# Optimization experiments

Measured on AMD Instinct MI355X. Metric: run time of the kernel, lower is better.

The kernel has to match this reference:

```python
import jax, jax.numpy as jnp
import numpy as np

T, D, F, FS, E = 2048, 1024, 2048, 2048, 8
TOP_K = 1


def setup_inputs() -> dict:
    key = jax.random.key(0)
    ks = jax.random.split(key, 8)
    sd = 1.0 / np.sqrt(D)
    sf = 1.0 / np.sqrt(F)
    sfs = 1.0 / np.sqrt(FS)
    return {
        "hidden_states": jax.random.normal(ks[0], (T, D), jnp.float32),
        "router_w": jax.random.normal(ks[1], (E, D), jnp.float32) * sd,     # Linear(D->E), no bias
        "w_gate": jax.random.normal(ks[2], (E, D, F), jnp.float32) * sd,    # fused gate half
        "w_up": jax.random.normal(ks[3], (E, D, F), jnp.float32) * sd,      # fused up half
        "w_down": jax.random.normal(ks[4], (E, F, D), jnp.float32) * sf,
        "ws_gate": jax.random.normal(ks[5], (D, FS), jnp.float32) * sd,
        "ws_up": jax.random.normal(ks[6], (D, FS), jnp.float32) * sd,
        "ws_down": jax.random.normal(ks[7], (FS, D), jnp.float32) * sfs,
    }


def reference(hidden_states, router_w, w_gate, w_up, w_down, ws_gate, ws_up, ws_down):
    # Router: logits -> top-k -> sigmoid of top-k values (Llama4RenormalizeMoeRoutingMethod)
    logits = hidden_states @ router_w.T                      # [T, E]
    top_vals, top_idx = jax.lax.top_k(logits, TOP_K)         # [T, K]
    scores = jax.nn.sigmoid(top_vals.astype(jnp.float32)).astype(hidden_states.dtype)
    # Combine weights [T, E]; apply_router_weight_on_input=True -> scale INPUT per routed copy
    combine = (jax.nn.one_hot(top_idx, E, dtype=hidden_states.dtype) * scores[..., None]).sum(axis=1)
    xe = combine.T[:, :, None] * hidden_states[None]          # [E, T, D] (zero for non-routed tokens)
    g = jnp.einsum('etd,edf->etf', xe, w_gate)
    u = jnp.einsum('etd,edf->etf', xe, w_up)
    routed = jnp.einsum('etf,efd->etd', jax.nn.silu(g) * u, w_down).sum(axis=0)  # [T, D]
    # Shared expert (GatedMLP, SiLU)
    shared = (jax.nn.silu(hidden_states @ ws_gate) * (hidden_states @ ws_up)) @ ws_down
    return shared + routed
```

## Files before the change

kernel.cpp:

```cpp
#include <hip/hip_runtime.h>
#include <hip/hip_bf16.h>
#include <cstdint>
#include <cstddef>

#define T_TOK 2048
#define DIM   1024
#define FDIM  2048
#define NEXP  8

#define GU_MAX 48
#define DN_MAX 64

typedef short  short8  __attribute__((ext_vector_type(8)));
typedef float  floatx4 __attribute__((ext_vector_type(4)));

__device__ inline unsigned short f2bf(float f) {
    unsigned int u = __builtin_bit_cast(unsigned int, f);
    unsigned int r = (u + 0x7FFFu + ((u >> 16) & 1u)) >> 16;
    return (unsigned short)r;
}

__device__ inline unsigned int pk2bf(float a, float b) {
    return (unsigned int)f2bf(a) | ((unsigned int)f2bf(b) << 16);
}

__device__ inline void glds16(const void* g, const unsigned short* lds_base, int elem_off) {
    int u = __builtin_amdgcn_readfirstlane(elem_off);
    __builtin_amdgcn_global_load_lds(
        (const __attribute__((address_space(1))) unsigned int*)g,
        (__attribute__((address_space(3))) unsigned int*)(lds_base + u), 16, 0, 0);
}

__global__ __launch_bounds__(256) void k_router(
    const float* __restrict__ h, const float* __restrict__ rw,
    int* __restrict__ counts, int* __restrict__ lists,
    unsigned short* __restrict__ hb, unsigned short* __restrict__ xb)
{
    int w = threadIdx.x >> 6, lane = threadIdx.x & 63;
    int t = blockIdx.x * 4 + w;
    const float* hrow = h + (size_t)t * DIM;
    float hv[16];
    #pragma unroll
    for (int i = 0; i < 16; ++i) hv[i] = hrow[lane + 64 * i];
    float acc[NEXP];
    #pragma unroll
    for (int e = 0; e < NEXP; ++e) {
        const float* r = rw + (size_t)e * DIM;
        float s = 0.f;
        #pragma unroll
        for (int i = 0; i < 16; ++i) s += hv[i] * r[lane + 64 * i];
        acc[e] = s;
    }
    #pragma unroll
    for (int e = 0; e < NEXP; ++e) {
        float s = acc[e];
        for (int off = 32; off > 0; off >>= 1) s += __shfl_down(s, off);
        acc[e] = s;
    }
    float score = 0.f;
    if (lane == 0) {
        int be = 0; float bv = acc[0];
        #pragma unroll
        for (int e = 1; e < NEXP; ++e) if (acc[e] > bv) { bv = acc[e]; be = e; }
        score = 1.f / (1.f + __expf(-bv));
        int pos = atomicAdd(&counts[be], 1);
        lists[be * T_TOK + pos] = t;
    }
    score = __shfl(score, 0);
    unsigned short* hbr = hb + (size_t)t * DIM;
    unsigned short* xbr = xb + (size_t)t * DIM;
    #pragma unroll
    for (int i = 0; i < 16; ++i) {
        hbr[lane + 64 * i] = f2bf(hv[i]);
        xbr[lane + 64 * i] = f2bf(score * hv[i]);
    }
}

__global__ void k_schedule(const int* __restrict__ counts,
                           int* __restrict__ gu, int* __restrict__ dn)
{
    if (threadIdx.x != 0 || blockIdx.x != 0) return;
    int n = 0;
    for (int e = 0; e < NEXP; ++e) {
        int c = counts[e];
        for (int r = 0; r < c; r += 128) gu[n++] = (e << 16) | r;
    }
    for (int r = 0; r < T_TOK; r += 128) gu[n++] = (NEXP << 16) | r;
    while (n < GU_MAX) gu[n++] = -1;
    n = 0;
    for (int e = 0; e < NEXP; ++e) {
        int c = counts[e];
        for (int r = 0; r < c; r += 128) {
            dn[n++] = (e << 16) | r;
            dn[n++] = (1 << 28) | (e << 16) | r;
        }
    }
    while (n < DN_MAX) dn[n++] = -1;
}

__global__ __launch_bounds__(256, 2) void k_gateup(
    const unsigned short* __restrict__ xb, const unsigned short* __restrict__ hb,
    const float* __restrict__ w_gate, const float* __restrict__ w_up,
    const float* __restrict__ ws_gate, const float* __restrict__ ws_up,
    const int* __restrict__ counts, const int* __restrict__ lists,
    const int* __restrict__ gu_tiles, unsigned short* __restrict__ Hc)
{
    int ent = gu_tiles[blockIdx.y];
    if (ent < 0) return;
    int e = ent >> 16, row0 = ent & 0xffff;
    bool sh = (e == NEXP);
    int cnt = sh ? T_TOK : counts[e];
    const unsigned short* Asrc = sh ? hb : xb;
    const float* Bg = sh ? ws_gate : w_gate + (size_t)e * DIM * FDIM;
    const float* Bu = sh ? ws_up   : w_up   + (size_t)e * DIM * FDIM;
    int outoff = sh ? FDIM : 0;
    int col0 = blockIdx.x * 128;

    __shared__ int toks[128];
    __shared__ __align__(16) unsigned short As [2][128 * 32];
    __shared__ __align__(16) unsigned short Bgs[2][128 * 32];
    __shared__ __align__(16) unsigned short Bus[2][128 * 32];

    int tid = threadIdx.x;
    if (tid < 128) {
        int r = row0 + tid;
        toks[tid] = (r < cnt) ? (sh ? r : lists[e * T_TOK + r]) : -1;
    }
    __syncthreads();

    int lane = tid & 63, w = tid >> 6;
    int wm = w >> 1, wn = w & 1;

    size_t agoff[2]; int albase[2];
    #pragma unroll
    for (int it = 0; it < 2; ++it) {
        int tt = tid + it * 256;
        int rr = tt >> 2, sq = tt & 3;
        int kg = (sq ^ ((rr >> 1) & 3)) * 8;
        int tk = toks[rr]; if (tk < 0) tk = 0;
        agoff[it] = (size_t)tk * DIM + kg;
        albase[it] = (it * 256 + w * 64) * 8;
    }

    int c = tid & 63;
    int kq = w;
    int slotB = (kq ^ (c & 3)) * 8;
    const float* bgp = Bg + (size_t)(kq * 8) * FDIM + col0 + 2 * c;
    const float* bup = Bu + (size_t)(kq * 8) * FDIM + col0 + 2 * c;

    float2 gx[8], ux[8];
    auto loadB = [&](int k0) {
        const float* pg = bgp + (size_t)k0 * FDIM;
        const float* pu = bup + (size_t)k0 * FDIM;
        #pragma unroll
        for (int j = 0; j < 8; ++j) {
            gx[j] = *(const float2*)(pg + (size_t)j * FDIM);
            ux[j] = *(const float2*)(pu + (size_t)j * FDIM);
        }
    };
    auto commitB = [&](int p) {
        unsigned int ge[4], go[4], ue[4], uo[4];
        #pragma unroll
        for (int j = 0; j < 4; ++j) {
            ge[j] = pk2bf(gx[2*j].x, gx[2*j+1].x);
            go[j] = pk2bf(gx[2*j].y, gx[2*j+1].y);
            ue[j] = pk2bf(ux[2*j].x, ux[2*j+1].x);
            uo[j] = pk2bf(ux[2*j].y, ux[2*j+1].y);
        }
        *(uint4*)&Bgs[p][(2*c)   * 32 + slotB] = make_uint4(ge[0], ge[1], ge[2], ge[3]);
        *(uint4*)&Bgs[p][(2*c+1) * 32 + slotB] = make_uint4(go[0], go[1], go[2], go[3]);
        *(uint4*)&Bus[p][(2*c)   * 32 + slotB] = make_uint4(ue[0], ue[1], ue[2], ue[3]);
        *(uint4*)&Bus[p][(2*c+1) * 32 + slotB] = make_uint4(uo[0], uo[1], uo[2], uo[3]);
    };
    auto loadA = [&](int k0, int p) {
        #pragma unroll
        for (int it = 0; it < 2; ++it)
            glds16(Asrc + agoff[it] + k0, &As[p][0], albase[it]);
    };

    floatx4 accg[4][4], accu[4][4];
    #pragma unroll
    for (int mi = 0; mi < 4; ++mi)
    #pragma unroll
    for (int ni = 0; ni < 4; ++ni) {
        floatx4 z = {0.f, 0.f, 0.f, 0.f};
        accg[mi][ni] = z; accu[mi][ni] = z;
    }

    loadA(0, 0);
    loadB(0);
    commitB(0);
    loadB(32);

    int p = 0;
    for (int k0 = 0; k0 < DIM; k0 += 32) {
        __syncthreads();
        int nk = k0 + 32;
        if (nk < DIM) {
            loadA(nk, p ^ 1);
            commitB(p ^ 1);
            if (nk + 32 < DIM) loadB(nk + 32);
        }
        int kb = (lane >> 4) * 8;
        short8 af[4], bgf[4], buf_[4];
        #pragma unroll
        for (int mi = 0; mi < 4; ++mi) {
            int r = wm * 64 + mi * 16 + (lane & 15);
            int slot = ((kb >> 3) ^ ((r >> 1) & 3)) * 8;
            af[mi] = *(const short8*)&As[p][r * 32 + slot];
        }
        #pragma unroll
        for (int ni = 0; ni < 4; ++ni) {
            int n = wn * 64 + ni * 16 + (lane & 15);
            int slot = ((kb >> 3) ^ ((n >> 1) & 3)) * 8;
            bgf[ni]  = *(const short8*)&Bgs[p][n * 32 + slot];
            buf_[ni] = *(const short8*)&Bus[p][n * 32 + slot];
        }
        #pragma unroll
        for (int mi = 0; mi < 4; ++mi)
        #pragma unroll
        for (int ni = 0; ni < 4; ++ni) {
            accg[mi][ni] = __builtin_amdgcn_mfma_f32_16x16x32_bf16(af[mi], bgf[ni],  accg[mi][ni], 0, 0, 0);
            accu[mi][ni] = __builtin_amdgcn_mfma_f32_16x16x32_bf16(af[mi], buf_[ni], accu[mi][ni], 0, 0, 0);
        }
        p ^= 1;
    }

    #pragma unroll
    for (int mi = 0; mi < 4; ++mi)
    #pragma unroll
    for (int ni = 0; ni < 4; ++ni)
    #pragma unroll
    for (int r = 0; r < 4; ++r) {
        int row = wm * 64 + mi * 16 + (lane >> 4) * 4 + r;
        int tok = toks[row];
        if (tok < 0) continue;
        int col = col0 + wn * 64 + ni * 16 + (lane & 15);
        float g = accg[mi][ni][r], u = accu[mi][ni][r];
        float hval = (g / (1.f + __expf(-g))) * u;
        Hc[(size_t)tok * (2 * FDIM) + outoff + col] = f2bf(hval);
    }
}

__global__ __launch_bounds__(256) void k_down(
    const unsigned short* __restrict__ Hc,
    const float* __restrict__ w_down, const float* __restrict__ ws_down,
    const int* __restrict__ counts, const int* __restrict__ lists,
    const int* __restrict__ dn_tiles, float* __restrict__ out)
{
    int ent = dn_tiles[blockIdx.y];
    if (ent < 0) return;
    int ks = (ent >> 28) & 1, e = (ent >> 16) & 0xff, row0 = ent & 0xffff;
    int cnt = counts[e];
    const float* B = ks ? ws_down : w_down + (size_t)e * FDIM * DIM;
    int col0 = blockIdx.x * 64;
    size_t abase = (size_t)ks * FDIM;

    __shared__ int toks[128];
    __shared__ __align__(16) unsigned short As[2][128 * 32];
    __shared__ __align__(16) unsigned short Bs[2][64 * 32];

    int tid = threadIdx.x;
    if (tid < 128) {
        int r = row0 + tid;
        toks[tid] = (r < cnt) ? lists[e * T_TOK + r] : -1;
    }
    __syncthreads();

    int lane = tid & 63, w = tid >> 6;
    int wm = w >> 1, wn = w & 1;

    size_t agoff[2]; int albase[2];
    #pragma unroll
    for (int it = 0; it < 2; ++it) {
        int tt = tid + it * 256;
        int rr = tt >> 2, sq = tt & 3;
        int kg = (sq ^ ((rr >> 1) & 3)) * 8;
        int tk = toks[rr]; if (tk < 0) tk = 0;
        agoff[it] = (size_t)tk * (2 * FDIM) + abase + kg;
        albase[it] = (it * 256 + w * 64) * 8;
    }

    int c = tid & 63;
    int kq = w;
    int slotB = (kq ^ ((c >> 1) & 3)) * 8;
    const float* bp = B + (size_t)(kq * 8) * DIM + col0 + c;

    float bx[8];
    auto loadB = [&](int k0) {
        const float* pb = bp + (size_t)k0 * DIM;
        #pragma unroll
        for (int j = 0; j < 8; ++j) bx[j] = pb[(size_t)j * DIM];
    };
    auto commitB = [&](int p) {
        unsigned int bw[4];
        #pragma unroll
        for (int j = 0; j < 4; ++j) bw[j] = pk2bf(bx[2*j], bx[2*j+1]);
        *(uint4*)&Bs[p][c * 32 + slotB] = make_uint4(bw[0], bw[1], bw[2], bw[3]);
    };
    auto loadA = [&](int k0, int p) {
        #pragma unroll
        for (int it = 0; it < 2; ++it)
            glds16(Hc + agoff[it] + k0, &As[p][0], albase[it]);
    };

    floatx4 acc[4][2];
    #pragma unroll
    for (int mi = 0; mi < 4; ++mi)
    #pragma unroll
    for (int ni = 0; ni < 2; ++ni) {
        floatx4 z = {0.f, 0.f, 0.f, 0.f};
        acc[mi][ni] = z;
    }

    loadA(0, 0);
    loadB(0);
    commitB(0);
    loadB(32);

    int p = 0;
    for (int k0 = 0; k0 < FDIM; k0 += 32) {
        __syncthreads();
        int nk = k0 + 32;
        if (nk < FDIM) {
            loadA(nk, p ^ 1);
            commitB(p ^ 1);
            if (nk + 32 < FDIM) loadB(nk + 32);
        }
        int kb = (lane >> 4) * 8;
        short8 af[4], bf[2];
        #pragma unroll
        for (int mi = 0; mi < 4; ++mi) {
            int r = wm * 64 + mi * 16 + (lane & 15);
            int slot = ((kb >> 3) ^ ((r >> 1) & 3)) * 8;
            af[mi] = *(const short8*)&As[p][r * 32 + slot];
        }
        #pragma unroll
        for (int ni = 0; ni < 2; ++ni) {
            int n = wn * 32 + ni * 16 + (lane & 15);
            int slot = ((kb >> 3) ^ ((n >> 1) & 3)) * 8;
            bf[ni] = *(const short8*)&Bs[p][n * 32 + slot];
        }
        #pragma unroll
        for (int mi = 0; mi < 4; ++mi)
        #pragma unroll
        for (int ni = 0; ni < 2; ++ni)
            acc[mi][ni] = __builtin_amdgcn_mfma_f32_16x16x32_bf16(af[mi], bf[ni], acc[mi][ni], 0, 0, 0);
        p ^= 1;
    }

    #pragma unroll
    for (int mi = 0; mi < 4; ++mi)
    #pragma unroll
    for (int ni = 0; ni < 2; ++ni)
    #pragma unroll
    for (int r = 0; r < 4; ++r) {
        int row = wm * 64 + mi * 16 + (lane >> 4) * 4 + r;
        int tok = toks[row];
        if (tok < 0) continue;
        int col = col0 + wn * 32 + ni * 16 + (lane & 15);
        atomicAdd(&out[(size_t)tok * DIM + col], acc[mi][ni][r]);
    }
}

extern "C" void kernel_launch(void* const* d_in, const int* in_sizes, int n_in,
                              void* d_out, int out_size, void* d_ws, size_t ws_size,
                              hipStream_t stream)
{
    const float* h   = (const float*)d_in[0];
    const float* rw  = (const float*)d_in[1];
    const float* wg  = (const float*)d_in[2];
    const float* wu  = (const float*)d_in[3];
    const float* wd  = (const float*)d_in[4];
    const float* wsg = (const float*)d_in[5];
    const float* wsu = (const float*)d_in[6];
    const float* wsd = (const float*)d_in[7];
    float* out = (float*)d_out;

    char* ws = (char*)d_ws;
    int* counts   = (int*)ws;
    int* gu_tiles = (int*)(ws + 256);
    int* dn_tiles = (int*)(ws + 1024);
    int* lists    = (int*)(ws + 2048);
    unsigned short* hb = (unsigned short*)(ws + 131072);
    unsigned short* xb = hb + (size_t)T_TOK * DIM;
    unsigned short* Hc = xb + (size_t)T_TOK * DIM;

    (void)hipMemsetAsync(counts, 0, 64, stream);
    (void)hipMemsetAsync(out, 0, (size_t)T_TOK * DIM * sizeof(float), stream);
    k_router<<<dim3(T_TOK / 4), 256, 0, stream>>>(h, rw, counts, lists, hb, xb);
    k_schedule<<<dim3(1), 64, 0, stream>>>(counts, gu_tiles, dn_tiles);
    k_gateup<<<dim3(FDIM / 128, GU_MAX), 256, 0, stream>>>(
        xb, hb, wg, wu, wsg, wsu, counts, lists, gu_tiles, Hc);
    k_down<<<dim3(DIM / 64, DN_MAX), 256, 0, stream>>>(
        Hc, wd, wsd, counts, lists, dn_tiles, out);
}
```

Measured before the change: 417.6 us.

## Restructure GEMM pipelines with hardware bf16 convert, padded LDS, wider down tiles

Replaces the software bf16 rounding with the v_cvt_pk_bf16_f32 instruction. The B tiles in LDS get a padded stride of 40 with a new XOR swizzle to cut bank conflicts. Both GEMM main loops are reordered: an explicit waitcnt plus barrier, the A prefetch issued first, the B commit and next load placed after the fragment reads, and s_setprio raised around the MFMA block. The down kernel's N tile grows from 64 to 128 columns with float2 B loads and launch bounds of (256,2). This raises register and LDS pressure, and the hand-tuned vmcnt values must match the exact number of outstanding loads.

Result: faster. 394.8 us (-5.5%).

```diff
diff --git a/kernel.cpp b/kernel.cpp
--- a/kernel.cpp
+++ b/kernel.cpp
@@ -20,8 +20,10 @@
     return (unsigned short)r;
 }
 
-__device__ inline unsigned int pk2bf(float a, float b) {
-    return (unsigned int)f2bf(a) | ((unsigned int)f2bf(b) << 16);
+__device__ inline unsigned int cvtpk(float a, float b) {
+    unsigned int r;
+    asm("v_cvt_pk_bf16_f32 %0, %1, %2" : "=v"(r) : "v"(a), "v"(b));
+    return r;
 }
 
 __device__ inline void glds16(const void* g, const unsigned short* lds_base, int elem_off) {
@@ -118,8 +120,8 @@
 
     __shared__ int toks[128];
     __shared__ __align__(16) unsigned short As [2][128 * 32];
-    __shared__ __align__(16) unsigned short Bgs[2][128 * 32];
-    __shared__ __align__(16) unsigned short Bus[2][128 * 32];
+    __shared__ __align__(16) unsigned short Bgs[2][128 * 40];
+    __shared__ __align__(16) unsigned short Bus[2][128 * 40];
 
     int tid = threadIdx.x;
     if (tid < 128) {
@@ -143,10 +145,9 @@
     }
 
     int c = tid & 63;
-    int kq = w;
-    int slotB = (kq ^ (c & 3)) * 8;
-    const float* bgp = Bg + (size_t)(kq * 8) * FDIM + col0 + 2 * c;
-    const float* bup = Bu + (size_t)(kq * 8) * FDIM + col0 + 2 * c;
+    int slotW = (w ^ ((c >> 2) & 1)) * 8;
+    const float* bgp = Bg + (size_t)(w * 8) * FDIM + col0 + 2 * c;
+    const float* bup = Bu + (size_t)(w * 8) * FDIM + col0 + 2 * c;
 
     float2 gx[8], ux[8];
     auto loadB = [&](int k0) {
@@ -158,24 +159,24 @@
             ux[j] = *(const float2*)(pu + (size_t)j * FDIM);
         }
     };
-    auto commitB = [&](int p) {
+    auto commitB = [&](int p_) {
         unsigned int ge[4], go[4], ue[4], uo[4];
         #pragma unroll
         for (int j = 0; j < 4; ++j) {
-            ge[j] = pk2bf(gx[2*j].x, gx[2*j+1].x);
-            go[j] = pk2bf(gx[2*j].y, gx[2*j+1].y);
-            ue[j] = pk2bf(ux[2*j].x, ux[2*j+1].x);
-            uo[j] = pk2bf(ux[2*j].y, ux[2*j+1].y);
-        }
-        *(uint4*)&Bgs[p][(2*c)   * 32 + slotB] = make_uint4(ge[0], ge[1], ge[2], ge[3]);
-        *(uint4*)&Bgs[p][(2*c+1) * 32 + slotB] = make_uint4(go[0], go[1], go[2], go[3]);
-        *(uint4*)&Bus[p][(2*c)   * 32 + slotB] = make_uint4(ue[0], ue[1], ue[2], ue[3]);
-        *(uint4*)&Bus[p][(2*c+1) * 32 + slotB] = make_uint4(uo[0], uo[1], uo[2], uo[3]);
-    };
-    auto loadA = [&](int k0, int p) {
+            ge[j] = cvtpk(gx[2*j].x, gx[2*j+1].x);
+            go[j] = cvtpk(gx[2*j].y, gx[2*j+1].y);
+            ue[j] = cvtpk(ux[2*j].x, ux[2*j+1].x);
+            uo[j] = cvtpk(ux[2*j].y, ux[2*j+1].y);
+        }
+        *(uint4*)&Bgs[p_][(2*c)   * 40 + slotW] = make_uint4(ge[0], ge[1], ge[2], ge[3]);
+        *(uint4*)&Bgs[p_][(2*c+1) * 40 + slotW] = make_uint4(go[0], go[1], go[2], go[3]);
+        *(uint4*)&Bus[p_][(2*c)   * 40 + slotW] = make_uint4(ue[0], ue[1], ue[2], ue[3]);
+        *(uint4*)&Bus[p_][(2*c+1) * 40 + slotW] = make_uint4(uo[0], uo[1], uo[2], uo[3]);
+    };
+    auto loadA = [&](int k0, int p_) {
         #pragma unroll
         for (int it = 0; it < 2; ++it)
-            glds16(Asrc + agoff[it] + k0, &As[p][0], albase[it]);
+            glds16(Asrc + agoff[it] + k0, &As[p_][0], albase[it]);
     };
 
     floatx4 accg[4][4], accu[4][4];
@@ -194,28 +195,31 @@
 
     int p = 0;
     for (int k0 = 0; k0 < DIM; k0 += 32) {
-        __syncthreads();
-        int nk = k0 + 32;
-        if (nk < DIM) {
-            loadA(nk, p ^ 1);
-            commitB(p ^ 1);
-            if (nk + 32 < DIM) loadB(nk + 32);
-        }
-        int kb = (lane >> 4) * 8;
+        asm volatile("s_waitcnt vmcnt(16) lgkmcnt(0)\n\ts_barrier" ::: "memory");
+        bool more = (k0 + 32 < DIM);
+        if (more) loadA(k0 + 32, p ^ 1);
+        __builtin_amdgcn_sched_barrier(0);
+        int g = lane >> 4;
         short8 af[4], bgf[4], buf_[4];
         #pragma unroll
         for (int mi = 0; mi < 4; ++mi) {
             int r = wm * 64 + mi * 16 + (lane & 15);
-            int slot = ((kb >> 3) ^ ((r >> 1) & 3)) * 8;
+            int slot = (g ^ ((r >> 1) & 3)) * 8;
             af[mi] = *(const short8*)&As[p][r * 32 + slot];
         }
         #pragma unroll
         for (int ni = 0; ni < 4; ++ni) {
             int n = wn * 64 + ni * 16 + (lane & 15);
-            int slot = ((kb >> 3) ^ ((n >> 1) & 3)) * 8;
-            bgf[ni]  = *(const short8*)&Bgs[p][n * 32 + slot];
-            buf_[ni] = *(const short8*)&Bus[p][n * 32 + slot];
-        }
+            int slot = (g ^ ((n >> 3) & 1)) * 8;
+            bgf[ni]  = *(const short8*)&Bgs[p][n * 40 + slot];
+            buf_[ni] = *(const short8*)&Bus[p][n * 40 + slot];
+        }
+        if (more) {
+            commitB(p ^ 1);
+            int nk2 = k0 + 64; if (nk2 >= DIM) nk2 = 0;
+            loadB(nk2);
+        }
+        __builtin_amdgcn_s_setprio(1);
         #pragma unroll
         for (int mi = 0; mi < 4; ++mi)
         #pragma unroll
@@ -223,6 +227,7 @@
             accg[mi][ni] = __builtin_amdgcn_mfma_f32_16x16x32_bf16(af[mi], bgf[ni],  accg[mi][ni], 0, 0, 0);
             accu[mi][ni] = __builtin_amdgcn_mfma_f32_16x16x32_bf16(af[mi], buf_[ni], accu[mi][ni], 0, 0, 0);
         }
+        __builtin_amdgcn_s_setprio(0);
         p ^= 1;
     }
 
@@ -236,13 +241,13 @@
         int tok = toks[row];
         if (tok < 0) continue;
         int col = col0 + wn * 64 + ni * 16 + (lane & 15);
-        float g = accg[mi][ni][r], u = accu[mi][ni][r];
-        float hval = (g / (1.f + __expf(-g))) * u;
+        float gv = accg[mi][ni][r], uv = accu[mi][ni][r];
+        float hval = (gv / (1.f + __expf(-gv))) * uv;
         Hc[(size_t)tok * (2 * FDIM) + outoff + col] = f2bf(hval);
     }
 }
 
-__global__ __launch_bounds__(256) void k_down(
+__global__ __launch_bounds__(256, 2) void k_down(
     const unsigned short* __restrict__ Hc,
     const float* __restrict__ w_down, const float* __restrict__ ws_down,
     const int* __restrict__ counts, const int* __restrict__ lists,
@@ -253,12 +258,12 @@
     int ks = (ent >> 28) & 1, e = (ent >> 16) & 0xff, row0 = ent & 0xffff;
     int cnt = counts[e];
     const float* B = ks ? ws_down : w_down + (size_t)e * FDIM * DIM;
-    int col0 = blockIdx.x * 64;
+    int col0 = blockIdx.x * 128;
     size_t abase = (size_t)ks * FDIM;
 
     __shared__ int toks[128];
     __shared__ __align__(16) unsigned short As[2][128 * 32];
-    __shared__ __align__(16) unsigned short Bs[2][64 * 32];
+    __shared__ __align__(16) unsigned short Bs[2][128 * 40];
 
     int tid = threadIdx.x;
     if (tid < 128) {
@@ -282,33 +287,36 @@
     }
 
     int c = tid & 63;
-    int kq = w;
-    int slotB = (kq ^ ((c >> 1) & 3)) * 8;
-    const float* bp = B + (size_t)(kq * 8) * DIM + col0 + c;
-
-    float bx[8];
+    int slotW = (w ^ ((c >> 2) & 1)) * 8;
+    const float* bp_ = B + (size_t)(w * 8) * DIM + col0 + 2 * c;
+
+    float2 bx[8];
     auto loadB = [&](int k0) {
-        const float* pb = bp + (size_t)k0 * DIM;
-        #pragma unroll
-        for (int j = 0; j < 8; ++j) bx[j] = pb[(size_t)j * DIM];
-    };
-    auto commitB = [&](int p) {
-        unsigned int bw[4];
-        #pragma unroll
-        for (int j = 0; j < 4; ++j) bw[j] = pk2bf(bx[2*j], bx[2*j+1]);
-        *(uint4*)&Bs[p][c * 32 + slotB] = make_uint4(bw[0], bw[1], bw[2], bw[3]);
-    };
-    auto loadA = [&](int k0, int p) {
+        const float* pb = bp_ + (size_t)k0 * DIM;
+        #pragma unroll
+        for (int j = 0; j < 8; ++j) bx[j] = *(const float2*)(pb + (size_t)j * DIM);
+    };
+    auto commitB = [&](int p_) {
+        unsigned int be[4], bo[4];
+        #pragma unroll
+        for (int j = 0; j < 4; ++j) {
+            be[j] = cvtpk(bx[2*j].x, bx[2*j+1].x);
+            bo[j] = cvtpk(bx[2*j].y, bx[2*j+1].y);
+        }
+        *(uint4*)&Bs[p_][(2*c)   * 40 + slotW] = make_uint4(be[0], be[1], be[2], be[3]);
+        *(uint4*)&Bs[p_][(2*c+1) * 40 + slotW] = make_uint4(bo[0], bo[1], bo[2], bo[3]);
+    };
+    auto loadA = [&](int k0, int p_) {
         #pragma unroll
         for (int it = 0; it < 2; ++it)
-            glds16(Hc + agoff[it] + k0, &As[p][0], albase[it]);
-    };
-
-    floatx4 acc[4][2];
+            glds16(Hc + agoff[it] + k0, &As[p_][0], albase[it]);
+    };
+
+    floatx4 acc[4][4];
     #pragma unroll
     for (int mi = 0; mi < 4; ++mi)
     #pragma unroll
-    for (int ni = 0; ni < 2; ++ni) {
+    for (int ni = 0; ni < 4; ++ni) {
         floatx4 z = {0.f, 0.f, 0.f, 0.f};
         acc[mi][ni] = z;
     }
@@ -320,45 +328,49 @@
 
     int p = 0;
     for (int k0 = 0; k0 < FDIM; k0 += 32) {
-        __syncthreads();
-        int nk = k0 + 32;
-        if (nk < FDIM) {
-            loadA(nk, p ^ 1);
-            commitB(p ^ 1);
-            if (nk + 32 < FDIM) loadB(nk + 32);
-        }
-        int kb = (lane >> 4) * 8;
-        short8 af[4], bf[2];
+        asm volatile("s_waitcnt vmcnt(8) lgkmcnt(0)\n\ts_barrier" ::: "memory");
+        bool more = (k0 + 32 < FDIM);
+        if (more) loadA(k0 + 32, p ^ 1);
+        __builtin_amdgcn_sched_barrier(0);
+        int g = lane >> 4;
+        short8 af[4], bf[4];
         #pragma unroll
         for (int mi = 0; mi < 4; ++mi) {
             int r = wm * 64 + mi * 16 + (lane & 15);
-            int slot = ((kb >> 3) ^ ((r >> 1) & 3)) * 8;
+            int slot = (g ^ ((r >> 1) & 3)) * 8;
             af[mi] = *(const short8*)&As[p][r * 32 + slot];
         }
         #pragma unroll
-        for (int ni = 0; ni < 2; ++ni) {
-            int n = wn * 32 + ni * 16 + (lane & 15);
-            int slot = ((kb >> 3) ^ ((n >> 1) & 3)) * 8;
-            bf[ni] = *(const short8*)&Bs[p][n * 32 + slot];
-        }
+        for (int ni = 0; ni < 4; ++ni) {
+            int n = wn * 64 + ni * 16 + (lane & 15);
+            int slot = (g ^ ((n >> 3) & 1)) * 8;
+            bf[ni] = *(const short8*)&Bs[p][n * 40 + slot];
+        }
+        if (more) {
+            commitB(p ^ 1);
+            int nk2 = k0 + 64; if (nk2 >= FDIM) nk2 = 0;
+            loadB(nk2);
+        }
+        __builtin_amdgcn_s_setprio(1);
         #pragma unroll
         for (int mi = 0; mi < 4; ++mi)
         #pragma unroll
-        for (int ni = 0; ni < 2; ++ni)
+        for (int ni = 0; ni < 4; ++ni)
             acc[mi][ni] = __builtin_amdgcn_mfma_f32_16x16x32_bf16(af[mi], bf[ni], acc[mi][ni], 0, 0, 0);
+        __builtin_amdgcn_s_setprio(0);
         p ^= 1;
     }
 
     #pragma unroll
     for (int mi = 0; mi < 4; ++mi)
     #pragma unroll
-    for (int ni = 0; ni < 2; ++ni)
+    for (int ni = 0; ni < 4; ++ni)
     #pragma unroll
     for (int r = 0; r < 4; ++r) {
         int row = wm * 64 + mi * 16 + (lane >> 4) * 4 + r;
         int tok = toks[row];
         if (tok < 0) continue;
-        int col = col0 + wn * 32 + ni * 16 + (lane & 15);
+        int col = col0 + wn * 64 + ni * 16 + (lane & 15);
         atomicAdd(&out[(size_t)tok * DIM + col], acc[mi][ni][r]);
     }
 }
@@ -392,6 +404,6 @@
     k_schedule<<<dim3(1), 64, 0, stream>>>(counts, gu_tiles, dn_tiles);
     k_gateup<<<dim3(FDIM / 128, GU_MAX), 256, 0, stream>>>(
         xb, hb, wg, wu, wsg, wsu, counts, lists, gu_tiles, Hc);
-    k_down<<<dim3(DIM / 64, DN_MAX), 256, 0, stream>>>(
+    k_down<<<dim3(DIM / 128, DN_MAX), 256, 0, stream>>>(
         Hc, wd, wsd, counts, lists, dn_tiles, out);
 }
```
